# Kernel optimization log

Measured on AMD Instinct MI355X. Metric: run time of the kernel, lower is better.

Reference implementation:

```python
import jax, jax.numpy as jnp
import numpy as np

EPS = 1e-12  # matches torch F.normalize eps


def _l2norm(v, axis):
    n = jnp.sqrt(jnp.sum(v * v, axis=axis, keepdims=True))
    return v / jnp.maximum(n, EPS)


def setup_inputs() -> dict:
    key = jax.random.key(0)
    k1, k2, k3, k4 = jax.random.split(key, 4)
    N, C, H, W, K = 64, 512, 40, 40, 64
    x = jax.random.normal(k1, (N, C, H, W), dtype=jnp.float32)
    conv_w = jax.random.normal(k2, (K, C), dtype=jnp.float32) * 0.05
    conv_b = jax.random.normal(k3, (K,), dtype=jnp.float32) * 0.05
    centroids = jax.random.uniform(k4, (K, C), dtype=jnp.float32)
    return {"x": x, "conv_w": conv_w, "conv_b": conv_b, "centroids": centroids}


def reference(x, conv_w, conv_b, centroids):
    N, C, H, W = x.shape
    K = centroids.shape[0]
    # descriptor-wise L2 normalization over channel dim
    x = _l2norm(x, axis=1)
    xf = x.reshape(N, C, H * W)                      # [N, C, M]
    # 1x1 conv == per-pixel linear: logits [N, K, M]
    logits = jnp.einsum('kc,ncm->nkm', conv_w, xf) + conv_b[None, :, None]
    a = jax.nn.softmax(logits, axis=1)               # softmax over clusters
    # vlad[n,k,c] = sum_m a[n,k,m] * (x[n,c,m] - cent[k,c])
    #            = (a @ x^T) - a_sum * cent   (avoids O(N*K*C*M) intermediate)
    agg = jnp.einsum('nkm,ncm->nkc', a, xf)          # [N, K, C]
    a_sum = jnp.sum(a, axis=2)                       # [N, K]
    vlad = agg - a_sum[:, :, None] * centroids[None, :, :]
    vlad = _l2norm(vlad, axis=2)                     # intra-normalization
    vlad = vlad.reshape(N, K * C)
    vlad = _l2norm(vlad, axis=1)                     # global L2 norm
    return vlad
```

## Files before the change

kernel.cpp:

```cpp
#include <hip/hip_runtime.h>
#include <hip/hip_bf16.h>

#define NN 64
#define CC 512
#define MM 1600
#define KK 64
#define EPSF 1e-12f

typedef __attribute__((ext_vector_type(4))) float f32x4;
typedef __attribute__((ext_vector_type(8))) short bf16x8;

__device__ inline unsigned short f2bf(float f) {
    __hip_bfloat16 b = __float2bfloat16(f);
    unsigned short u;
    __builtin_memcpy(&u, &b, sizeof(u));
    return u;
}

__global__ __launch_bounds__(256) void wconv_kernel(
    const float* __restrict__ w, unsigned short* __restrict__ wb)
{
    const int i = (blockIdx.x * 256 + threadIdx.x) * 8;
    float4 a = *(const float4*)(w + i);
    float4 b = *(const float4*)(w + i + 4);
    ushort4 u0, u1;
    u0.x = f2bf(a.x); u0.y = f2bf(a.y); u0.z = f2bf(a.z); u0.w = f2bf(a.w);
    u1.x = f2bf(b.x); u1.y = f2bf(b.y); u1.z = f2bf(b.z); u1.w = f2bf(b.w);
    *(ushort4*)(wb + i) = u0;
    *(ushort4*)(wb + i + 4) = u1;
}

__global__ __launch_bounds__(64) void fused1_kernel(
    const float* __restrict__ x, const unsigned short* __restrict__ wb,
    const float* __restrict__ bias,
    unsigned short* __restrict__ ap, float* __restrict__ asum_part)
{
    const int t  = threadIdx.x;
    const int n  = blockIdx.y;
    const int mtile = blockIdx.x;
    const int m0   = mtile * 64;
    const int g    = t >> 4;
    const int lr   = t & 15;

    f32x4 acc[4][4];
    #pragma unroll
    for (int kt = 0; kt < 4; ++kt)
        #pragma unroll
        for (int j = 0; j < 4; ++j) acc[kt][j] = (f32x4){0.f, 0.f, 0.f, 0.f};
    float ss0 = 0.f, ss1 = 0.f, ss2 = 0.f, ss3 = 0.f;

    const float* xcol = x + (size_t)n * CC * MM + m0 + 4 * lr;
    const unsigned short* wrow = wb + g * 8;

    float4 xv[2][8];
    #pragma unroll
    for (int j8 = 0; j8 < 8; ++j8)
        xv[0][j8] = *(const float4*)(xcol + (size_t)(g * 8 + j8) * MM);

    #pragma unroll
    for (int cs = 0; cs < 16; ++cs) {
        const int cur = cs & 1;
        if (cs < 15) {
            #pragma unroll
            for (int j8 = 0; j8 < 8; ++j8)
                xv[cur ^ 1][j8] = *(const float4*)(
                    xcol + (size_t)((cs + 1) * 32 + g * 8 + j8) * MM);
        }
        bf16x8 bfrag0, bfrag1, bfrag2, bfrag3;
        #pragma unroll
        for (int j8 = 0; j8 < 8; ++j8) {
            const float4 v = xv[cur][j8];
            ss0 += v.x * v.x; ss1 += v.y * v.y;
            ss2 += v.z * v.z; ss3 += v.w * v.w;
            bfrag0[j8] = (short)f2bf(v.x);
            bfrag1[j8] = (short)f2bf(v.y);
            bfrag2[j8] = (short)f2bf(v.z);
            bfrag3[j8] = (short)f2bf(v.w);
        }
        #pragma unroll
        for (int kt = 0; kt < 4; ++kt) {
            bf16x8 afrag = *(const bf16x8*)(wrow + (kt * 16 + lr) * CC + cs * 32);
            acc[kt][0] = __builtin_amdgcn_mfma_f32_16x16x32_bf16(afrag, bfrag0, acc[kt][0], 0, 0, 0);
            acc[kt][1] = __builtin_amdgcn_mfma_f32_16x16x32_bf16(afrag, bfrag1, acc[kt][1], 0, 0, 0);
            acc[kt][2] = __builtin_amdgcn_mfma_f32_16x16x32_bf16(afrag, bfrag2, acc[kt][2], 0, 0, 0);
            acc[kt][3] = __builtin_amdgcn_mfma_f32_16x16x32_bf16(afrag, bfrag3, acc[kt][3], 0, 0, 0);
        }
    }

    float rnm[4];
    {
        ss0 += __shfl_xor(ss0, 16); ss0 += __shfl_xor(ss0, 32);
        ss1 += __shfl_xor(ss1, 16); ss1 += __shfl_xor(ss1, 32);
        ss2 += __shfl_xor(ss2, 16); ss2 += __shfl_xor(ss2, 32);
        ss3 += __shfl_xor(ss3, 16); ss3 += __shfl_xor(ss3, 32);
        rnm[0] = 1.0f / fmaxf(sqrtf(ss0), EPSF);
        rnm[1] = 1.0f / fmaxf(sqrtf(ss1), EPSF);
        rnm[2] = 1.0f / fmaxf(sqrtf(ss2), EPSF);
        rnm[3] = 1.0f / fmaxf(sqrtf(ss3), EPSF);
    }

    #pragma unroll
    for (int kt = 0; kt < 4; ++kt) {
        float4 bb = *(const float4*)(bias + kt * 16 + g * 4);
        #pragma unroll
        for (int j = 0; j < 4; ++j) {
            acc[kt][j][0] = acc[kt][j][0] * rnm[j] + bb.x;
            acc[kt][j][1] = acc[kt][j][1] * rnm[j] + bb.y;
            acc[kt][j][2] = acc[kt][j][2] * rnm[j] + bb.z;
            acc[kt][j][3] = acc[kt][j][3] * rnm[j] + bb.w;
        }
    }

    float inv[4];
    #pragma unroll
    for (int j = 0; j < 4; ++j) {
        float mx = acc[0][j][0];
        #pragma unroll
        for (int kt = 0; kt < 4; ++kt)
            #pragma unroll
            for (int r = 0; r < 4; ++r) mx = fmaxf(mx, acc[kt][j][r]);
        mx = fmaxf(mx, __shfl_xor(mx, 16));
        mx = fmaxf(mx, __shfl_xor(mx, 32));
        float s = 0.f;
        #pragma unroll
        for (int kt = 0; kt < 4; ++kt)
            #pragma unroll
            for (int r = 0; r < 4; ++r) {
                float e = __expf(acc[kt][j][r] - mx);
                acc[kt][j][r] = e;
                s += e;
            }
        s += __shfl_xor(s, 16);
        s += __shfl_xor(s, 32);
        inv[j] = 1.0f / s;
    }

    float asum_acc[16];
    #pragma unroll
    for (int kt = 0; kt < 4; ++kt)
        #pragma unroll
        for (int r = 0; r < 4; ++r) {
            const float a0 = acc[kt][0][r] * inv[0];
            const float a1 = acc[kt][1][r] * inv[1];
            const float a2 = acc[kt][2][r] * inv[2];
            const float a3 = acc[kt][3][r] * inv[3];
            asum_acc[kt * 4 + r] = (a0 + a1) + (a2 + a3);
            ushort4 u;
            u.x = f2bf(a0 * rnm[0]);
            u.y = f2bf(a1 * rnm[1]);
            u.z = f2bf(a2 * rnm[2]);
            u.w = f2bf(a3 * rnm[3]);
            const int k = kt * 16 + g * 4 + r;
            *(ushort4*)(ap + ((size_t)(n * KK + k)) * MM + m0 + 4 * lr) = u;
        }

    #pragma unroll
    for (int i = 0; i < 16; ++i) {
        asum_acc[i] += __shfl_xor(asum_acc[i], 1);
        asum_acc[i] += __shfl_xor(asum_acc[i], 2);
        asum_acc[i] += __shfl_xor(asum_acc[i], 4);
        asum_acc[i] += __shfl_xor(asum_acc[i], 8);
    }
    if (lr == 0) {
        #pragma unroll
        for (int kt = 0; kt < 4; ++kt)
            #pragma unroll
            for (int r = 0; r < 4; ++r)
                asum_part[((size_t)(n * 25 + mtile)) * 64 + kt * 16 + g * 4 + r]
                    = asum_acc[kt * 4 + r];
    }
}

__global__ __launch_bounds__(256) void aggm_kernel(
    const float* __restrict__ x, const unsigned short* __restrict__ ap,
    float* __restrict__ aggp)
{
    __shared__ __attribute__((aligned(16))) unsigned short als2[64][72];
    const int t    = threadIdx.x;
    const int ct   = blockIdx.x;
    const int mh   = blockIdx.y;
    const int n    = blockIdx.z;
    const int wv   = t >> 6;
    const int lane = t & 63;
    const int g    = lane >> 4;
    const int lr   = lane & 15;
    const int c_w  = ct * 64 + wv * 16;

    f32x4 acc[4];
    #pragma unroll
    for (int kt = 0; kt < 4; ++kt) acc[kt] = (f32x4){0.f, 0.f, 0.f, 0.f};

    const int ks = t >> 2, qs = t & 3;
    const float* xrow = x + ((size_t)(n * CC + c_w + lr)) * MM;

    const int mc_beg = mh ? 832 : 0;
    const int mc_end = mh ? MM : 832;

    for (int mc = mc_beg; mc < mc_end; mc += 64) {
        __syncthreads();
        {
            const unsigned short* src = ap + ((size_t)(n * KK + ks)) * MM + mc + qs * 16;
            uint4 w0 = *(const uint4*)src;
            uint4 w1 = *(const uint4*)(src + 8);
            *(uint4*)&als2[ks][qs * 16] = w0;
            *(uint4*)&als2[ks][qs * 16 + 8] = w1;
        }
        __syncthreads();
        #pragma unroll
        for (int msi = 0; msi < 2; ++msi) {
            const int ms = msi * 32;
            float4 v0 = *(const float4*)(xrow + mc + ms + g * 8);
            float4 v1 = *(const float4*)(xrow + mc + ms + g * 8 + 4);
            bf16x8 bf;
            bf[0] = (short)f2bf(v0.x); bf[1] = (short)f2bf(v0.y);
            bf[2] = (short)f2bf(v0.z); bf[3] = (short)f2bf(v0.w);
            bf[4] = (short)f2bf(v1.x); bf[5] = (short)f2bf(v1.y);
            bf[6] = (short)f2bf(v1.z); bf[7] = (short)f2bf(v1.w);
            #pragma unroll
            for (int kt = 0; kt < 4; ++kt) {
                bf16x8 af = *(const bf16x8*)&als2[kt * 16 + lr][ms + g * 8];
                acc[kt] = __builtin_amdgcn_mfma_f32_16x16x32_bf16(af, bf, acc[kt], 0, 0, 0);
            }
        }
    }
    #pragma unroll
    for (int kt = 0; kt < 4; ++kt)
        #pragma unroll
        for (int r = 0; r < 4; ++r) {
            const int k = kt * 16 + g * 4 + r;
            aggp[((size_t)((mh * NN + n) * KK + k)) * CC + c_w + lr] = acc[kt][r];
        }
}

__global__ __launch_bounds__(256) void vlad_kernel(
    const float* __restrict__ aggp, const float* __restrict__ asum_part,
    const float* __restrict__ cent, float* __restrict__ out)
{
    __shared__ float wsum[4];
    __shared__ float sinv;
    const int nk = blockIdx.x;
    const int n = nk >> 6, k = nk & 63;
    const int t = threadIdx.x;
    const int u = t & 63;
    const size_t half = (size_t)NN * KK * CC;

    float pa = (u < 25) ? asum_part[((size_t)(n * 25 + u)) * 64 + k] : 0.f;
    #pragma unroll
    for (int o = 32; o > 0; o >>= 1) pa += __shfl_xor(pa, o);
    const float s = pa;

    float2 a0 = *(const float2*)(aggp + (size_t)nk * CC + 2 * t);
    float2 a1 = *(const float2*)(aggp + half + (size_t)nk * CC + 2 * t);
    float2 cv = *(const float2*)(cent + (size_t)k * CC + 2 * t);
    float v0 = (a0.x + a1.x) - s * cv.x;
    float v1 = (a0.y + a1.y) - s * cv.y;
    float ss = v0 * v0 + v1 * v1;
    #pragma unroll
    for (int o = 32; o > 0; o >>= 1) ss += __shfl_down(ss, o);
    int wid = t >> 6;
    if (u == 0) wsum[wid] = ss;
    __syncthreads();
    if (t == 0) {
        float tot = wsum[0] + wsum[1] + wsum[2] + wsum[3];
        sinv = 1.0f / fmaxf(sqrtf(tot), EPSF);
    }
    __syncthreads();
    const float sc = sinv * 0.125f;
    float2 o2; o2.x = v0 * sc; o2.y = v1 * sc;
    *(float2*)(out + (size_t)nk * CC + 2 * t) = o2;
}

extern "C" void kernel_launch(void* const* d_in, const int* in_sizes, int n_in,
                              void* d_out, int out_size, void* d_ws, size_t ws_size,
                              hipStream_t stream)
{
    const float* x    = (const float*)d_in[0];
    const float* w    = (const float*)d_in[1];
    const float* bias = (const float*)d_in[2];
    const float* cent = (const float*)d_in[3];
    float* out = (float*)d_out;

    char* ws = (char*)d_ws;
    size_t off = 0;
    unsigned short* ap  = (unsigned short*)(ws + off); off += (size_t)NN * KK * MM * 2;
    unsigned short* wb  = (unsigned short*)(ws + off); off += (size_t)KK * CC * 2;
    float* aggp      = (float*)(ws + off); off += (size_t)2 * NN * KK * CC * 4;
    float* asum_part = (float*)(ws + off); off += (size_t)NN * 25 * KK * 4;

    wconv_kernel <<<16, 256, 0, stream>>>(w, wb);
    fused1_kernel<<<dim3(25, 64), 64, 0, stream>>>(x, wb, bias, ap, asum_part);
    aggm_kernel  <<<dim3(8, 2, 64), 256, 0, stream>>>(x, ap, aggp);
    vlad_kernel  <<<NN * KK, 256, 0, stream>>>(aggp, asum_part, cent, out);
}
```

Baseline: 98.32 us.

## Switch logits kernel to 32x32x16 MFMA with 128-pixel tiles

Reworks the first fused kernel to use 32x32x16 bf16 MFMA instructions and process 128 pixels per wavefront instead of 64, halving the grid to 13 tiles per image with masking for the ragged last tile. Each weight fragment load now feeds more pixel columns, which cuts redundant weight traffic and per-tile overhead. The costs are fewer blocks (13x64 single-wave blocks, which may underfill the GPU), larger accumulator register pressure, and wasted work in the partially valid last tile. The softmax, normalization and asum reductions are remapped to the new accumulator layout.

```diff
diff --git a/kernel.cpp b/kernel.cpp
--- a/kernel.cpp
+++ b/kernel.cpp
@@ -6,8 +6,10 @@
 #define MM 1600
 #define KK 64
 #define EPSF 1e-12f
+#define NT1 13
 
 typedef __attribute__((ext_vector_type(4))) float f32x4;
+typedef __attribute__((ext_vector_type(16))) float f32x16;
 typedef __attribute__((ext_vector_type(8))) short bf16x8;
 
 __device__ inline unsigned short f2bf(float f) {
@@ -35,139 +37,147 @@
     const float* __restrict__ bias,
     unsigned short* __restrict__ ap, float* __restrict__ asum_part)
 {
-    const int t  = threadIdx.x;
-    const int n  = blockIdx.y;
-    const int mtile = blockIdx.x;
-    const int m0   = mtile * 64;
-    const int g    = t >> 4;
-    const int lr   = t & 15;
-
-    f32x4 acc[4][4];
-    #pragma unroll
-    for (int kt = 0; kt < 4; ++kt)
-        #pragma unroll
-        for (int j = 0; j < 4; ++j) acc[kt][j] = (f32x4){0.f, 0.f, 0.f, 0.f};
+    const int t    = threadIdx.x;
+    const int n    = blockIdx.y;
+    const int tile = blockIdx.x;
+    const int m0   = tile * 128;
+    const int c31  = t & 31;
+    const int h    = t >> 5;
+
+    const int  mcol   = m0 + 4 * c31;
+    const bool mvalid = mcol < MM;
+    const int  mld    = mvalid ? mcol : (MM - 4);
+
+    f32x16 acc[2][4];
+    #pragma unroll
+    for (int kt = 0; kt < 2; ++kt)
+        #pragma unroll
+        for (int j = 0; j < 4; ++j)
+            #pragma unroll
+            for (int r = 0; r < 16; ++r) acc[kt][j][r] = 0.f;
     float ss0 = 0.f, ss1 = 0.f, ss2 = 0.f, ss3 = 0.f;
 
-    const float* xcol = x + (size_t)n * CC * MM + m0 + 4 * lr;
-    const unsigned short* wrow = wb + g * 8;
+    const float* xcol = x + (size_t)n * CC * MM + mld;
 
     float4 xv[2][8];
     #pragma unroll
     for (int j8 = 0; j8 < 8; ++j8)
-        xv[0][j8] = *(const float4*)(xcol + (size_t)(g * 8 + j8) * MM);
-
-    #pragma unroll
-    for (int cs = 0; cs < 16; ++cs) {
+        xv[0][j8] = *(const float4*)(xcol + (size_t)(h * 8 + j8) * MM);
+
+    #pragma unroll
+    for (int cs = 0; cs < 32; ++cs) {
         const int cur = cs & 1;
-        if (cs < 15) {
+        if (cs < 31) {
             #pragma unroll
             for (int j8 = 0; j8 < 8; ++j8)
                 xv[cur ^ 1][j8] = *(const float4*)(
-                    xcol + (size_t)((cs + 1) * 32 + g * 8 + j8) * MM);
-        }
-        bf16x8 bfrag0, bfrag1, bfrag2, bfrag3;
+                    xcol + (size_t)((cs + 1) * 16 + h * 8 + j8) * MM);
+        }
+        bf16x8 bf0, bf1, bf2, bf3;
         #pragma unroll
         for (int j8 = 0; j8 < 8; ++j8) {
             const float4 v = xv[cur][j8];
             ss0 += v.x * v.x; ss1 += v.y * v.y;
             ss2 += v.z * v.z; ss3 += v.w * v.w;
-            bfrag0[j8] = (short)f2bf(v.x);
-            bfrag1[j8] = (short)f2bf(v.y);
-            bfrag2[j8] = (short)f2bf(v.z);
-            bfrag3[j8] = (short)f2bf(v.w);
-        }
-        #pragma unroll
-        for (int kt = 0; kt < 4; ++kt) {
-            bf16x8 afrag = *(const bf16x8*)(wrow + (kt * 16 + lr) * CC + cs * 32);
-            acc[kt][0] = __builtin_amdgcn_mfma_f32_16x16x32_bf16(afrag, bfrag0, acc[kt][0], 0, 0, 0);
-            acc[kt][1] = __builtin_amdgcn_mfma_f32_16x16x32_bf16(afrag, bfrag1, acc[kt][1], 0, 0, 0);
-            acc[kt][2] = __builtin_amdgcn_mfma_f32_16x16x32_bf16(afrag, bfrag2, acc[kt][2], 0, 0, 0);
-            acc[kt][3] = __builtin_amdgcn_mfma_f32_16x16x32_bf16(afrag, bfrag3, acc[kt][3], 0, 0, 0);
+            bf0[j8] = (short)f2bf(v.x);
+            bf1[j8] = (short)f2bf(v.y);
+            bf2[j8] = (short)f2bf(v.z);
+            bf3[j8] = (short)f2bf(v.w);
+        }
+        #pragma unroll
+        for (int kt = 0; kt < 2; ++kt) {
+            bf16x8 afrag = *(const bf16x8*)(
+                wb + (size_t)(kt * 32 + c31) * CC + cs * 16 + h * 8);
+            acc[kt][0] = __builtin_amdgcn_mfma_f32_32x32x16_bf16(afrag, bf0, acc[kt][0], 0, 0, 0);
+            acc[kt][1] = __builtin_amdgcn_mfma_f32_32x32x16_bf16(afrag, bf1, acc[kt][1], 0, 0, 0);
+            acc[kt][2] = __builtin_amdgcn_mfma_f32_32x32x16_bf16(afrag, bf2, acc[kt][2], 0, 0, 0);
+            acc[kt][3] = __builtin_amdgcn_mfma_f32_32x32x16_bf16(afrag, bf3, acc[kt][3], 0, 0, 0);
         }
     }
 
     float rnm[4];
-    {
-        ss0 += __shfl_xor(ss0, 16); ss0 += __shfl_xor(ss0, 32);
-        ss1 += __shfl_xor(ss1, 16); ss1 += __shfl_xor(ss1, 32);
-        ss2 += __shfl_xor(ss2, 16); ss2 += __shfl_xor(ss2, 32);
-        ss3 += __shfl_xor(ss3, 16); ss3 += __shfl_xor(ss3, 32);
-        rnm[0] = 1.0f / fmaxf(sqrtf(ss0), EPSF);
-        rnm[1] = 1.0f / fmaxf(sqrtf(ss1), EPSF);
-        rnm[2] = 1.0f / fmaxf(sqrtf(ss2), EPSF);
-        rnm[3] = 1.0f / fmaxf(sqrtf(ss3), EPSF);
-    }
-
-    #pragma unroll
-    for (int kt = 0; kt < 4; ++kt) {
-        float4 bb = *(const float4*)(bias + kt * 16 + g * 4);
-        #pragma unroll
-        for (int j = 0; j < 4; ++j) {
-            acc[kt][j][0] = acc[kt][j][0] * rnm[j] + bb.x;
-            acc[kt][j][1] = acc[kt][j][1] * rnm[j] + bb.y;
-            acc[kt][j][2] = acc[kt][j][2] * rnm[j] + bb.z;
-            acc[kt][j][3] = acc[kt][j][3] * rnm[j] + bb.w;
-        }
-    }
+    ss0 += __shfl_xor(ss0, 32);
+    ss1 += __shfl_xor(ss1, 32);
+    ss2 += __shfl_xor(ss2, 32);
+    ss3 += __shfl_xor(ss3, 32);
+    rnm[0] = 1.0f / fmaxf(sqrtf(ss0), EPSF);
+    rnm[1] = 1.0f / fmaxf(sqrtf(ss1), EPSF);
+    rnm[2] = 1.0f / fmaxf(sqrtf(ss2), EPSF);
+    rnm[3] = 1.0f / fmaxf(sqrtf(ss3), EPSF);
+
+    #pragma unroll
+    for (int kt = 0; kt < 2; ++kt)
+        #pragma unroll
+        for (int rr = 0; rr < 4; ++rr) {
+            const float4 bb = *(const float4*)(bias + kt * 32 + 8 * rr + 4 * h);
+            #pragma unroll
+            for (int j = 0; j < 4; ++j) {
+                acc[kt][j][rr * 4 + 0] = acc[kt][j][rr * 4 + 0] * rnm[j] + bb.x;
+                acc[kt][j][rr * 4 + 1] = acc[kt][j][rr * 4 + 1] * rnm[j] + bb.y;
+                acc[kt][j][rr * 4 + 2] = acc[kt][j][rr * 4 + 2] * rnm[j] + bb.z;
+                acc[kt][j][rr * 4 + 3] = acc[kt][j][rr * 4 + 3] * rnm[j] + bb.w;
+            }
+        }
 
     float inv[4];
     #pragma unroll
     for (int j = 0; j < 4; ++j) {
         float mx = acc[0][j][0];
         #pragma unroll
-        for (int kt = 0; kt < 4; ++kt)
-            #pragma unroll
-            for (int r = 0; r < 4; ++r) mx = fmaxf(mx, acc[kt][j][r]);
-        mx = fmaxf(mx, __shfl_xor(mx, 16));
+        for (int kt = 0; kt < 2; ++kt)
+            #pragma unroll
+            for (int r = 0; r < 16; ++r) mx = fmaxf(mx, acc[kt][j][r]);
         mx = fmaxf(mx, __shfl_xor(mx, 32));
         float s = 0.f;
         #pragma unroll
-        for (int kt = 0; kt < 4; ++kt)
-            #pragma unroll
-            for (int r = 0; r < 4; ++r) {
-                float e = __expf(acc[kt][j][r] - mx);
+        for (int kt = 0; kt < 2; ++kt)
+            #pragma unroll
+            for (int r = 0; r < 16; ++r) {
+                const float e = __expf(acc[kt][j][r] - mx);
                 acc[kt][j][r] = e;
                 s += e;
             }
-        s += __shfl_xor(s, 16);
         s += __shfl_xor(s, 32);
         inv[j] = 1.0f / s;
     }
 
-    float asum_acc[16];
-    #pragma unroll
-    for (int kt = 0; kt < 4; ++kt)
-        #pragma unroll
-        for (int r = 0; r < 4; ++r) {
-            const float a0 = acc[kt][0][r] * inv[0];
-            const float a1 = acc[kt][1][r] * inv[1];
-            const float a2 = acc[kt][2][r] * inv[2];
-            const float a3 = acc[kt][3][r] * inv[3];
-            asum_acc[kt * 4 + r] = (a0 + a1) + (a2 + a3);
-            ushort4 u;
-            u.x = f2bf(a0 * rnm[0]);
-            u.y = f2bf(a1 * rnm[1]);
-            u.z = f2bf(a2 * rnm[2]);
-            u.w = f2bf(a3 * rnm[3]);
-            const int k = kt * 16 + g * 4 + r;
-            *(ushort4*)(ap + ((size_t)(n * KK + k)) * MM + m0 + 4 * lr) = u;
-        }
-
-    #pragma unroll
-    for (int i = 0; i < 16; ++i) {
+    float asum_acc[32];
+    #pragma unroll
+    for (int kt = 0; kt < 2; ++kt)
+        #pragma unroll
+        for (int reg = 0; reg < 16; ++reg) {
+            const float a0 = acc[kt][0][reg] * inv[0];
+            const float a1 = acc[kt][1][reg] * inv[1];
+            const float a2 = acc[kt][2][reg] * inv[2];
+            const float a3 = acc[kt][3][reg] * inv[3];
+            asum_acc[kt * 16 + reg] = mvalid ? ((a0 + a1) + (a2 + a3)) : 0.f;
+            if (mvalid) {
+                ushort4 u;
+                u.x = f2bf(a0 * rnm[0]);
+                u.y = f2bf(a1 * rnm[1]);
+                u.z = f2bf(a2 * rnm[2]);
+                u.w = f2bf(a3 * rnm[3]);
+                const int k = kt * 32 + (reg & 3) + 8 * (reg >> 2) + 4 * h;
+                *(ushort4*)(ap + ((size_t)(n * KK + k)) * MM + mcol) = u;
+            }
+        }
+
+    #pragma unroll
+    for (int i = 0; i < 32; ++i) {
         asum_acc[i] += __shfl_xor(asum_acc[i], 1);
         asum_acc[i] += __shfl_xor(asum_acc[i], 2);
         asum_acc[i] += __shfl_xor(asum_acc[i], 4);
         asum_acc[i] += __shfl_xor(asum_acc[i], 8);
-    }
-    if (lr == 0) {
-        #pragma unroll
-        for (int kt = 0; kt < 4; ++kt)
-            #pragma unroll
-            for (int r = 0; r < 4; ++r)
-                asum_part[((size_t)(n * 25 + mtile)) * 64 + kt * 16 + g * 4 + r]
-                    = asum_acc[kt * 4 + r];
+        asum_acc[i] += __shfl_xor(asum_acc[i], 16);
+    }
+    if (c31 == 0) {
+        float* dst = asum_part + ((size_t)(n * NT1 + tile)) * 64;
+        #pragma unroll
+        for (int kt = 0; kt < 2; ++kt)
+            #pragma unroll
+            for (int reg = 0; reg < 16; ++reg)
+                dst[kt * 32 + (reg & 3) + 8 * (reg >> 2) + 4 * h]
+                    = asum_acc[kt * 16 + reg];
     }
 }
 
@@ -244,7 +254,7 @@
     const int u = t & 63;
     const size_t half = (size_t)NN * KK * CC;
 
-    float pa = (u < 25) ? asum_part[((size_t)(n * 25 + u)) * 64 + k] : 0.f;
+    float pa = (u < NT1) ? asum_part[((size_t)(n * NT1 + u)) * 64 + k] : 0.f;
     #pragma unroll
     for (int o = 32; o > 0; o >>= 1) pa += __shfl_xor(pa, o);
     const float s = pa;
@@ -285,10 +295,10 @@
     unsigned short* ap  = (unsigned short*)(ws + off); off += (size_t)NN * KK * MM * 2;
     unsigned short* wb  = (unsigned short*)(ws + off); off += (size_t)KK * CC * 2;
     float* aggp      = (float*)(ws + off); off += (size_t)2 * NN * KK * CC * 4;
-    float* asum_part = (float*)(ws + off); off += (size_t)NN * 25 * KK * 4;
+    float* asum_part = (float*)(ws + off); off += (size_t)NN * NT1 * KK * 4;
 
     wconv_kernel <<<16, 256, 0, stream>>>(w, wb);
-    fused1_kernel<<<dim3(25, 64), 64, 0, stream>>>(x, wb, bias, ap, asum_part);
+    fused1_kernel<<<dim3(NT1, 64), 64, 0, stream>>>(x, wb, bias, ap, asum_part);
     aggm_kernel  <<<dim3(8, 2, 64), 256, 0, stream>>>(x, ap, aggp);
     vlad_kernel  <<<NN * KK, 256, 0, stream>>>(aggp, asum_part, cent, out);
 }
```

New measurement: 102.1 us. +3.9%, slower.

## Precompute bf16 copy of x and per-pixel sum of squares in a prep kernel

Applied to the files above, without the earlier changes.

Adds a prep kernel that converts x to bf16 once and writes partial per-pixel sums of squares, then the logits and aggregation kernels read the bf16 copy instead of converting fp32 on the fly. This removes duplicated fp32-to-bf16 conversion and norm work from two kernels and halves their x read size. In exchange it adds an extra full write of a bf16 copy of x plus its reread, raising total memory traffic, and adds a kernel launch.

```diff
diff --git a/kernel.cpp b/kernel.cpp
--- a/kernel.cpp
+++ b/kernel.cpp
@@ -30,9 +30,36 @@
     *(ushort4*)(wb + i + 4) = u1;
 }
 
-__global__ __launch_bounds__(64) void fused1_kernel(
-    const float* __restrict__ x, const unsigned short* __restrict__ wb,
-    const float* __restrict__ bias,
+__global__ __launch_bounds__(512) void prep_kernel(
+    const float* __restrict__ x, unsigned short* __restrict__ xb,
+    float* __restrict__ rnp)
+{
+    const int t  = threadIdx.x;
+    if (t >= 400) return;
+    const int cchunk = blockIdx.x;
+    const int n      = blockIdx.y;
+    const int m4 = t * 4;
+
+    float s0 = 0.f, s1 = 0.f, s2 = 0.f, s3 = 0.f;
+    const size_t base = (size_t)(n * CC + cchunk * 64) * MM + m4;
+    const float* xp = x + base;
+    unsigned short* xo = xb + base;
+
+    #pragma unroll 4
+    for (int cc = 0; cc < 64; ++cc) {
+        float4 v = *(const float4*)(xp + (size_t)cc * MM);
+        s0 += v.x * v.x; s1 += v.y * v.y; s2 += v.z * v.z; s3 += v.w * v.w;
+        ushort4 b;
+        b.x = f2bf(v.x); b.y = f2bf(v.y); b.z = f2bf(v.z); b.w = f2bf(v.w);
+        *(ushort4*)(xo + (size_t)cc * MM) = b;
+    }
+    float4 ssv; ssv.x = s0; ssv.y = s1; ssv.z = s2; ssv.w = s3;
+    *(float4*)(rnp + (size_t)(n * 8 + cchunk) * MM + m4) = ssv;
+}
+
+__global__ __launch_bounds__(64) void logits_kernel(
+    const unsigned short* __restrict__ xb, const float* __restrict__ rnp,
+    const unsigned short* __restrict__ wb, const float* __restrict__ bias,
     unsigned short* __restrict__ ap, float* __restrict__ asum_part)
 {
     const int t  = threadIdx.x;
@@ -47,15 +74,14 @@
     for (int kt = 0; kt < 4; ++kt)
         #pragma unroll
         for (int j = 0; j < 4; ++j) acc[kt][j] = (f32x4){0.f, 0.f, 0.f, 0.f};
-    float ss0 = 0.f, ss1 = 0.f, ss2 = 0.f, ss3 = 0.f;
-
-    const float* xcol = x + (size_t)n * CC * MM + m0 + 4 * lr;
+
+    const unsigned short* xcol = xb + (size_t)n * CC * MM + m0 + 4 * lr;
     const unsigned short* wrow = wb + g * 8;
 
-    float4 xv[2][8];
+    ushort4 xv[2][8];
     #pragma unroll
     for (int j8 = 0; j8 < 8; ++j8)
-        xv[0][j8] = *(const float4*)(xcol + (size_t)(g * 8 + j8) * MM);
+        xv[0][j8] = *(const ushort4*)(xcol + (size_t)(g * 8 + j8) * MM);
 
     #pragma unroll
     for (int cs = 0; cs < 16; ++cs) {
@@ -63,19 +89,17 @@
         if (cs < 15) {
             #pragma unroll
             for (int j8 = 0; j8 < 8; ++j8)
-                xv[cur ^ 1][j8] = *(const float4*)(
+                xv[cur ^ 1][j8] = *(const ushort4*)(
                     xcol + (size_t)((cs + 1) * 32 + g * 8 + j8) * MM);
         }
         bf16x8 bfrag0, bfrag1, bfrag2, bfrag3;
         #pragma unroll
         for (int j8 = 0; j8 < 8; ++j8) {
-            const float4 v = xv[cur][j8];
-            ss0 += v.x * v.x; ss1 += v.y * v.y;
-            ss2 += v.z * v.z; ss3 += v.w * v.w;
-            bfrag0[j8] = (short)f2bf(v.x);
-            bfrag1[j8] = (short)f2bf(v.y);
-            bfrag2[j8] = (short)f2bf(v.z);
-            bfrag3[j8] = (short)f2bf(v.w);
+            const ushort4 v = xv[cur][j8];
+            bfrag0[j8] = (short)v.x;
+            bfrag1[j8] = (short)v.y;
+            bfrag2[j8] = (short)v.z;
+            bfrag3[j8] = (short)v.w;
         }
         #pragma unroll
         for (int kt = 0; kt < 4; ++kt) {
@@ -88,15 +112,13 @@
     }
 
     float rnm[4];
-    {
-        ss0 += __shfl_xor(ss0, 16); ss0 += __shfl_xor(ss0, 32);
-        ss1 += __shfl_xor(ss1, 16); ss1 += __shfl_xor(ss1, 32);
-        ss2 += __shfl_xor(ss2, 16); ss2 += __shfl_xor(ss2, 32);
-        ss3 += __shfl_xor(ss3, 16); ss3 += __shfl_xor(ss3, 32);
-        rnm[0] = 1.0f / fmaxf(sqrtf(ss0), EPSF);
-        rnm[1] = 1.0f / fmaxf(sqrtf(ss1), EPSF);
-        rnm[2] = 1.0f / fmaxf(sqrtf(ss2), EPSF);
-        rnm[3] = 1.0f / fmaxf(sqrtf(ss3), EPSF);
+    #pragma unroll
+    for (int j = 0; j < 4; ++j) {
+        const float* rp = rnp + (size_t)n * 8 * MM + m0 + 4 * lr + j;
+        float ss = 0.f;
+        #pragma unroll
+        for (int p = 0; p < 8; ++p) ss += rp[(size_t)p * MM];
+        rnm[j] = 1.0f / fmaxf(sqrtf(ss), EPSF);
     }
 
     #pragma unroll
@@ -172,7 +194,7 @@
 }
 
 __global__ __launch_bounds__(256) void aggm_kernel(
-    const float* __restrict__ x, const unsigned short* __restrict__ ap,
+    const unsigned short* __restrict__ xb, const unsigned short* __restrict__ ap,
     float* __restrict__ aggp)
 {
     __shared__ __attribute__((aligned(16))) unsigned short als2[64][72];
@@ -191,7 +213,7 @@
     for (int kt = 0; kt < 4; ++kt) acc[kt] = (f32x4){0.f, 0.f, 0.f, 0.f};
 
     const int ks = t >> 2, qs = t & 3;
-    const float* xrow = x + ((size_t)(n * CC + c_w + lr)) * MM;
+    const unsigned short* xrow = xb + ((size_t)(n * CC + c_w + lr)) * MM;
 
     const int mc_beg = mh ? 832 : 0;
     const int mc_end = mh ? MM : 832;
@@ -209,13 +231,7 @@
         #pragma unroll
         for (int msi = 0; msi < 2; ++msi) {
             const int ms = msi * 32;
-            float4 v0 = *(const float4*)(xrow + mc + ms + g * 8);
-            float4 v1 = *(const float4*)(xrow + mc + ms + g * 8 + 4);
-            bf16x8 bf;
-            bf[0] = (short)f2bf(v0.x); bf[1] = (short)f2bf(v0.y);
-            bf[2] = (short)f2bf(v0.z); bf[3] = (short)f2bf(v0.w);
-            bf[4] = (short)f2bf(v1.x); bf[5] = (short)f2bf(v1.y);
-            bf[6] = (short)f2bf(v1.z); bf[7] = (short)f2bf(v1.w);
+            bf16x8 bf = *(const bf16x8*)(xrow + mc + ms + g * 8);
             #pragma unroll
             for (int kt = 0; kt < 4; ++kt) {
                 bf16x8 af = *(const bf16x8*)&als2[kt * 16 + lr][ms + g * 8];
@@ -282,13 +298,16 @@
 
     char* ws = (char*)d_ws;
     size_t off = 0;
+    unsigned short* xb  = (unsigned short*)(ws + off); off += (size_t)NN * CC * MM * 2;
     unsigned short* ap  = (unsigned short*)(ws + off); off += (size_t)NN * KK * MM * 2;
     unsigned short* wb  = (unsigned short*)(ws + off); off += (size_t)KK * CC * 2;
+    float* rnp       = (float*)(ws + off); off += (size_t)NN * 8 * MM * 4;
     float* aggp      = (float*)(ws + off); off += (size_t)2 * NN * KK * CC * 4;
     float* asum_part = (float*)(ws + off); off += (size_t)NN * 25 * KK * 4;
 
     wconv_kernel <<<16, 256, 0, stream>>>(w, wb);
-    fused1_kernel<<<dim3(25, 64), 64, 0, stream>>>(x, wb, bias, ap, asum_part);
-    aggm_kernel  <<<dim3(8, 2, 64), 256, 0, stream>>>(x, ap, aggp);
+    prep_kernel  <<<dim3(8, 64), 512, 0, stream>>>(x, xb, rnp);
+    logits_kernel<<<dim3(25, 64), 64, 0, stream>>>(xb, rnp, wb, bias, ap, asum_part);
+    aggm_kernel  <<<dim3(8, 2, 64), 256, 0, stream>>>(xb, ap, aggp);
     vlad_kernel  <<<NN * KK, 256, 0, stream>>>(aggp, asum_part, cent, out);
 }
```

Result: slower. 137.3 us (+39.7%).
